# Kernel tuning notes

Measured on AMD Instinct MI355X. Metric: run time of the kernel, lower is better.

The kernel has to match this reference:

```python
import jax, jax.numpy as jnp
import numpy as np

B, D_IN, HID, DEPTH = 16384, 128, 16, 8
N_INNER = 2 ** DEPTH - 1   # 255
N_LEAF = 2 ** DEPTH        # 256


def setup_inputs() -> dict:
    key = jax.random.key(0)
    ks = jax.random.split(key, 4)
    x = jax.random.normal(ks[0], (B, D_IN), jnp.float32)
    # Batched per-inner-node tiny MLP parameters (PyTorch stores one Sequential per node;
    # we stack them along a leading node axis so the math is identical but vectorized).
    W1 = jax.random.normal(ks[1], (N_INNER, D_IN, HID), jnp.float32) / np.sqrt(D_IN).astype(np.float32)
    b1 = jnp.zeros((N_INNER, HID), jnp.float32)
    W2 = jax.random.normal(ks[2], (N_INNER, HID), jnp.float32) / np.sqrt(HID).astype(np.float32)
    b2 = jnp.zeros((N_INNER,), jnp.float32)
    leaf = jax.random.normal(ks[3], (N_LEAF, 1), jnp.float32) * 0.1
    return {"x": x, "W1": W1, "b1": b1, "W2": W2, "b2": b2, "leaf": leaf}


def reference(x, W1, b1, W2, b2, leaf):
    b = x.shape[0]
    depth = int(np.log2(leaf.shape[0]))
    # All inner-node gates in one batched GEMM: p[b, n] = sigmoid(W2_n . relu(W1_n^T x_b + b1_n) + b2_n)
    h1 = jax.nn.relu(jnp.einsum('bi,nih->bnh', x, W1) + b1[None])  # [B, N_inner, hid]
    p = jax.nn.sigmoid(jnp.einsum('bnh,nh->bn', h1, W2) + b2[None])  # [B, N_inner]

    # Level-by-level probability propagation (heap-ordered nodes):
    # children of node j are 2j+1 (left, mass*(1-p)) and 2j+2 (right, mass*p).
    r = jnp.ones((b, 1), x.dtype)
    levels = []
    for l in range(depth):
        levels.append(r)
        pl = p[:, 2 ** l - 1: 2 ** (l + 1) - 1]  # probs of nodes at level l, [B, 2^l]
        # interleave (left, right) so child ordering matches heap indexing
        r = jnp.stack([r * (1.0 - pl), r * pl], axis=-1).reshape(b, 2 ** (l + 1))
    node_reach = jnp.concatenate(levels, axis=1)  # [B, N_inner]
    path_probs = r                                 # [B, N_leaf]

    h = (path_probs @ leaf)[:, 0]                  # [B]
    return (h, path_probs, p, node_reach)
```

## Files before the change

### kernel.cpp

```cpp
#include <hip/hip_runtime.h>

#define BATCH 16384
#define DIN   128
#define HIDN  16
#define NNODE 255
#define NLEAF 256

typedef _Float16 half8 __attribute__((ext_vector_type(8)));
typedef float   float4v __attribute__((ext_vector_type(4)));

__global__ __launch_bounds__(256) void k_pack_x(const float* __restrict__ x, half8* __restrict__ xp) {
    int gid  = blockIdx.x * 256 + threadIdx.x;
    int lane = gid & 63;
    int kc   = (gid >> 6) & 3;
    int bt   = gid >> 8;
    const float4* src = (const float4*)(x + (size_t)(bt * 16 + (lane & 15)) * DIN + kc * 32 + ((lane >> 4) * 8));
    float4 v0 = src[0], v1 = src[1];
    half8 v;
    v[0] = (_Float16)v0.x; v[1] = (_Float16)v0.y; v[2] = (_Float16)v0.z; v[3] = (_Float16)v0.w;
    v[4] = (_Float16)v1.x; v[5] = (_Float16)v1.y; v[6] = (_Float16)v1.z; v[7] = (_Float16)v1.w;
    xp[gid] = v;
}

__global__ __launch_bounds__(256) void k_pack_w1(const float* __restrict__ w1, half8* __restrict__ w1p) {
    __shared__ float w[DIN * 17];
    int n = blockIdx.x;
    int t = threadIdx.x;
    const float4* src = (const float4*)(w1 + (size_t)n * (DIN * HIDN)) + t * 2;
    float4 a0 = src[0], a1 = src[1];
    int base = t * 8;
#pragma unroll
    for (int e = 0; e < 4; ++e) {
        int idx0 = base + e, idx1 = base + 4 + e;
        float v0 = (&a0.x)[e], v1 = (&a1.x)[e];
        w[(idx0 >> 4) * 17 + (idx0 & 15)] = v0;
        w[(idx1 >> 4) * 17 + (idx1 & 15)] = v1;
    }
    __syncthreads();
    int L  = t & 63;
    int kc = t >> 6;
    int m  = L & 15;
    int k0 = kc * 32 + (L >> 4) * 8;
    half8 v;
#pragma unroll
    for (int j = 0; j < 8; ++j) v[j] = (_Float16)w[(k0 + j) * 17 + m];
    w1p[(size_t)n * 256 + t] = v;
}

__global__ __launch_bounds__(256, 4) void k_mlp(const half8* __restrict__ xp, const half8* __restrict__ w1p,
                                                const float* __restrict__ b1, const float* __restrict__ w2,
                                                const float* __restrict__ b2, float* __restrict__ p_ws) {
    int wave = threadIdx.x >> 6;
    int lane = threadIdx.x & 63;
    int q    = lane >> 4;
    int c    = lane & 15;
    int bt0  = blockIdx.x * 16 + wave * 4;
    int n0   = blockIdx.y * 15;

    half8 bq[4][4];
#pragma unroll
    for (int t = 0; t < 4; ++t)
#pragma unroll
        for (int kc = 0; kc < 4; ++kc)
            bq[t][kc] = xp[(size_t)((bt0 + t) * 4 + kc) * 64 + lane];
    asm volatile("" ::: "memory");

    for (int i = 0; i < 15; ++i) {
        int n = n0 + i;
        half8 a[4];
#pragma unroll
        for (int kc = 0; kc < 4; ++kc) a[kc] = w1p[(size_t)(n * 4 + kc) * 64 + lane];
        float4 b1f = ((const float4*)(b1 + n * HIDN))[q];
        float4 w2f = ((const float4*)(w2 + n * HIDN))[q];
        float  b2v = b2[n];
#pragma unroll
        for (int t = 0; t < 4; ++t) {
            float4v acc = {b1f.x, b1f.y, b1f.z, b1f.w};
#pragma unroll
            for (int kc = 0; kc < 4; ++kc)
                acc = __builtin_amdgcn_mfma_f32_16x16x32_f16(a[kc], bq[t][kc], acc, 0, 0, 0);
            float s = fmaf(fmaxf(acc[0], 0.f), w2f.x,
                      fmaf(fmaxf(acc[1], 0.f), w2f.y,
                      fmaf(fmaxf(acc[2], 0.f), w2f.z,
                           fmaxf(acc[3], 0.f) * w2f.w)));
            s += __shfl_xor(s, 16, 64);
            s += __shfl_xor(s, 32, 64);
            float logit = s + b2v;
            float pv = __builtin_amdgcn_rcpf(1.f + __builtin_amdgcn_exp2f(-1.44269504088896f * logit));
            if (lane < 16)
                p_ws[(size_t)n * BATCH + (bt0 + t) * 16 + c] = pv;
        }
    }
}

__global__ __launch_bounds__(256) void k_tree(const float* __restrict__ p_ws, const float* __restrict__ leaf,
                                              float* __restrict__ h_out, float* __restrict__ pp_out,
                                              float* __restrict__ p_out, float* __restrict__ nr_out) {
    __shared__ float sp[32][NNODE + 2];
    int wv   = threadIdx.x >> 6;
    int lane = threadIdx.x & 63;
    int b0   = blockIdx.x * 32;
    int t    = threadIdx.x;

    for (int i = 0; i < 32; ++i) {
        int idx = i * 256 + t;
        if (idx < NNODE * 32) {
            int n = idx >> 5, bl = idx & 31;
            sp[bl][n] = p_ws[(size_t)n * BATCH + b0 + bl];
        }
    }
    __syncthreads();

    for (int r = 0; r < 32; ++r)
        if (t < NNODE)
            p_out[(size_t)(b0 + r) * NNODE + t] = sp[r][t];

    for (int rr = 0; rr < 8; ++rr) {
        int i = wv * 8 + rr;
        int b = b0 + i;
        const float* P = &sp[i][0];
        float* nr = nr_out + (size_t)b * NNODE;

        float pref = 1.f;
#pragma unroll
        for (int l = 0; l < 6; ++l) {
            if ((lane & ((1 << (6 - l)) - 1)) == 0) nr[(1 << l) - 1 + (lane >> (6 - l))] = pref;
            float pv  = P[(1 << l) - 1 + (lane >> (6 - l))];
            int  bit  = (lane >> (5 - l)) & 1;
            pref *= bit ? pv : (1.f - pv);
        }
        nr[63 + lane] = pref;
        float p6 = P[63 + lane];
        float pl = pref * (1.f - p6);
        float pr = pref * p6;
        nr[127 + 2 * lane] = pl;
        nr[128 + 2 * lane] = pr;
        float p7a = P[127 + 2 * lane];
        float p7b = P[128 + 2 * lane];
        float4 pp;
        pp.x = pl * (1.f - p7a);
        pp.y = pl * p7a;
        pp.z = pr * (1.f - p7b);
        pp.w = pr * p7b;
        *(float4*)(pp_out + (size_t)b * NLEAF + 4 * lane) = pp;
        const float4 lf = *(const float4*)(leaf + 4 * lane);
        float hs = pp.x * lf.x + pp.y * lf.y + pp.z * lf.z + pp.w * lf.w;
#pragma unroll
        for (int off = 1; off < 64; off <<= 1) hs += __shfl_xor(hs, off, 64);
        if (lane == 0) h_out[b] = hs;
    }
}

extern "C" void kernel_launch(void* const* d_in, const int* in_sizes, int n_in,
                              void* d_out, int out_size, void* d_ws, size_t ws_size,
                              hipStream_t stream) {
    const float* x    = (const float*)d_in[0];
    const float* W1   = (const float*)d_in[1];
    const float* b1   = (const float*)d_in[2];
    const float* W2   = (const float*)d_in[3];
    const float* b2   = (const float*)d_in[4];
    const float* leaf = (const float*)d_in[5];

    float* out    = (float*)d_out;
    float* h_out  = out;
    float* pp_out = out + BATCH;
    float* p_out  = pp_out + (size_t)BATCH * NLEAF;
    float* nr_out = p_out + (size_t)BATCH * NNODE;

    half8* xp   = (half8*)d_ws;
    half8* w1p  = xp + (size_t)1024 * 4 * 64;
    float* p_ws = (float*)(w1p + (size_t)NNODE * 256);

    hipLaunchKernelGGL(k_pack_x,  dim3(1024),  dim3(256), 0, stream, x, xp);
    hipLaunchKernelGGL(k_pack_w1, dim3(NNODE), dim3(256), 0, stream, W1, w1p);
    hipLaunchKernelGGL(k_mlp,     dim3(64, 17), dim3(256), 0, stream, xp, w1p, b1, W2, b2, p_ws);
    hipLaunchKernelGGL(k_tree,    dim3(BATCH / 32), dim3(256), 0, stream,
                       p_ws, leaf, h_out, pp_out, p_out, nr_out);
}
```

Before: 133.0 us.

## Swap MFMA operand roles, DPP row reductions, move sigmoid to tree kernel, smaller tiles

k_mlp swaps the MFMA A/B operands so each lane holds four batch rows for one hidden unit. The W2 dot product becomes a DPP row reduction over 16 lanes, replacing cross-row shuffles, and each row writes a float4 of logits. Each wave now handles 2 batch tiles instead of 4, the grid doubles, and launch bounds rise to 5 blocks per CU. The sigmoid moves into k_tree, which now works on 16 rows per block, doubling its grid and shrinking shared memory to raise parallelism. The trade-off is more redundant W1 loads per batch tile and more blocks to schedule.

```diff
diff --git a/kernel.cpp b/kernel.cpp
--- a/kernel.cpp
+++ b/kernel.cpp
@@ -5,9 +5,19 @@
 #define HIDN  16
 #define NNODE 255
 #define NLEAF 256
+#define TR    16
 
 typedef _Float16 half8 __attribute__((ext_vector_type(8)));
 typedef float   float4v __attribute__((ext_vector_type(4)));
+
+__device__ __forceinline__ float row_reduce16(float x) {
+    union U { float f; int i; } u, v;
+    u.f = x; v.i = __builtin_amdgcn_update_dpp(0, u.i, 0x128, 0xF, 0xF, true); x += v.f;
+    u.f = x; v.i = __builtin_amdgcn_update_dpp(0, u.i, 0x124, 0xF, 0xF, true); x += v.f;
+    u.f = x; v.i = __builtin_amdgcn_update_dpp(0, u.i, 0x122, 0xF, 0xF, true); x += v.f;
+    u.f = x; v.i = __builtin_amdgcn_update_dpp(0, u.i, 0x121, 0xF, 0xF, true); x += v.f;
+    return x;
+}
 
 __global__ __launch_bounds__(256) void k_pack_x(const float* __restrict__ x, half8* __restrict__ xp) {
     int gid  = blockIdx.x * 256 + threadIdx.x;
@@ -47,48 +57,50 @@
     w1p[(size_t)n * 256 + t] = v;
 }
 
-__global__ __launch_bounds__(256, 4) void k_mlp(const half8* __restrict__ xp, const half8* __restrict__ w1p,
+__global__ __launch_bounds__(256, 5) void k_mlp(const half8* __restrict__ xp, const half8* __restrict__ w1p,
                                                 const float* __restrict__ b1, const float* __restrict__ w2,
                                                 const float* __restrict__ b2, float* __restrict__ p_ws) {
-    int wave = threadIdx.x >> 6;
+    int wv   = threadIdx.x >> 6;
     int lane = threadIdx.x & 63;
-    int q    = lane >> 4;
-    int c    = lane & 15;
-    int bt0  = blockIdx.x * 16 + wave * 4;
+    int rg   = lane >> 4;
+    int hc   = lane & 15;
+    int bt0  = blockIdx.x * 8 + wv * 2;
     int n0   = blockIdx.y * 15;
 
-    half8 bq[4][4];
+    half8 xa[2][4];
 #pragma unroll
-    for (int t = 0; t < 4; ++t)
+    for (int t = 0; t < 2; ++t)
 #pragma unroll
         for (int kc = 0; kc < 4; ++kc)
-            bq[t][kc] = xp[(size_t)((bt0 + t) * 4 + kc) * 64 + lane];
+            xa[t][kc] = xp[(size_t)((bt0 + t) * 4 + kc) * 64 + lane];
     asm volatile("" ::: "memory");
 
     for (int i = 0; i < 15; ++i) {
         int n = n0 + i;
-        half8 a[4];
+        half8 wb[4];
 #pragma unroll
-        for (int kc = 0; kc < 4; ++kc) a[kc] = w1p[(size_t)(n * 4 + kc) * 64 + lane];
-        float4 b1f = ((const float4*)(b1 + n * HIDN))[q];
-        float4 w2f = ((const float4*)(w2 + n * HIDN))[q];
-        float  b2v = b2[n];
+        for (int kc = 0; kc < 4; ++kc) wb[kc] = w1p[(size_t)(n * 4 + kc) * 64 + lane];
+        float b1v = b1[n * HIDN + hc];
+        float w2v = w2[n * HIDN + hc];
+        float b2v = b2[n];
 #pragma unroll
-        for (int t = 0; t < 4; ++t) {
-            float4v acc = {b1f.x, b1f.y, b1f.z, b1f.w};
+        for (int t = 0; t < 2; ++t) {
+            float4v acc = {b1v, b1v, b1v, b1v};
 #pragma unroll
             for (int kc = 0; kc < 4; ++kc)
-                acc = __builtin_amdgcn_mfma_f32_16x16x32_f16(a[kc], bq[t][kc], acc, 0, 0, 0);
-            float s = fmaf(fmaxf(acc[0], 0.f), w2f.x,
-                      fmaf(fmaxf(acc[1], 0.f), w2f.y,
-                      fmaf(fmaxf(acc[2], 0.f), w2f.z,
-                           fmaxf(acc[3], 0.f) * w2f.w)));
-            s += __shfl_xor(s, 16, 64);
-            s += __shfl_xor(s, 32, 64);
-            float logit = s + b2v;
-            float pv = __builtin_amdgcn_rcpf(1.f + __builtin_amdgcn_exp2f(-1.44269504088896f * logit));
-            if (lane < 16)
-                p_ws[(size_t)n * BATCH + (bt0 + t) * 16 + c] = pv;
+                acc = __builtin_amdgcn_mfma_f32_16x16x32_f16(xa[t][kc], wb[kc], acc, 0, 0, 0);
+            float s0 = fmaxf(acc[0], 0.f) * w2v;
+            float s1 = fmaxf(acc[1], 0.f) * w2v;
+            float s2 = fmaxf(acc[2], 0.f) * w2v;
+            float s3 = fmaxf(acc[3], 0.f) * w2v;
+            s0 = row_reduce16(s0);
+            s1 = row_reduce16(s1);
+            s2 = row_reduce16(s2);
+            s3 = row_reduce16(s3);
+            if (hc == 0) {
+                float4 o = {s0 + b2v, s1 + b2v, s2 + b2v, s3 + b2v};
+                *(float4*)(p_ws + (size_t)n * BATCH + (bt0 + t) * 16 + rg * 4) = o;
+            }
         }
     }
 }
@@ -96,27 +108,29 @@
 __global__ __launch_bounds__(256) void k_tree(const float* __restrict__ p_ws, const float* __restrict__ leaf,
                                               float* __restrict__ h_out, float* __restrict__ pp_out,
                                               float* __restrict__ p_out, float* __restrict__ nr_out) {
-    __shared__ float sp[32][NNODE + 2];
+    __shared__ float sp[TR][NNODE + 2];
     int wv   = threadIdx.x >> 6;
     int lane = threadIdx.x & 63;
-    int b0   = blockIdx.x * 32;
+    int b0   = blockIdx.x * TR;
     int t    = threadIdx.x;
 
-    for (int i = 0; i < 32; ++i) {
+#pragma unroll
+    for (int i = 0; i < 16; ++i) {
         int idx = i * 256 + t;
-        if (idx < NNODE * 32) {
-            int n = idx >> 5, bl = idx & 31;
-            sp[bl][n] = p_ws[(size_t)n * BATCH + b0 + bl];
+        if (idx < NNODE * TR) {
+            int n = idx >> 4, bl = idx & 15;
+            float lg = p_ws[(size_t)n * BATCH + b0 + bl];
+            sp[bl][n] = __builtin_amdgcn_rcpf(1.f + __builtin_amdgcn_exp2f(-1.44269504088896f * lg));
         }
     }
     __syncthreads();
 
-    for (int r = 0; r < 32; ++r)
+    for (int r = 0; r < TR; ++r)
         if (t < NNODE)
             p_out[(size_t)(b0 + r) * NNODE + t] = sp[r][t];
 
-    for (int rr = 0; rr < 8; ++rr) {
-        int i = wv * 8 + rr;
+    for (int rr = 0; rr < 4; ++rr) {
+        int i = wv * 4 + rr;
         int b = b0 + i;
         const float* P = &sp[i][0];
         float* nr = nr_out + (size_t)b * NNODE;
@@ -173,7 +187,7 @@
 
     hipLaunchKernelGGL(k_pack_x,  dim3(1024),  dim3(256), 0, stream, x, xp);
     hipLaunchKernelGGL(k_pack_w1, dim3(NNODE), dim3(256), 0, stream, W1, w1p);
-    hipLaunchKernelGGL(k_mlp,     dim3(64, 17), dim3(256), 0, stream, xp, w1p, b1, W2, b2, p_ws);
-    hipLaunchKernelGGL(k_tree,    dim3(BATCH / 32), dim3(256), 0, stream,
+    hipLaunchKernelGGL(k_mlp,     dim3(128, 17), dim3(256), 0, stream, xp, w1p, b1, W2, b2, p_ws);
+    hipLaunchKernelGGL(k_tree,    dim3(BATCH / TR), dim3(256), 0, stream,
                        p_ws, leaf, h_out, pp_out, p_out, nr_out);
 }
```

Result: no change. 131.5 us (-1.1%).

## Merge pack kernels, use MFMA for second layer, move sigmoid into tree kernel

Applied to the files above, without the earlier changes.

Merges the x and W1 packing kernels into one launch, which also converts W2 to fp16. The second MLP layer's reduction (relu times W2 plus two cross-lane shuffles) becomes a 16x16x16 fp16 MFMA seeded with b2, and the kernel now stores raw logits. The sigmoid moves into the tree kernel's load phase, and that kernel now handles 16 rows per block instead of 32, doubling the block count. The MFMA path rounds the ReLU activations and W2 to fp16, which adds precision loss.

```diff
diff --git a/kernel.cpp b/kernel.cpp
--- a/kernel.cpp
+++ b/kernel.cpp
@@ -5,56 +5,60 @@
 #define HIDN  16
 #define NNODE 255
 #define NLEAF 256
+#define TR    16
 
 typedef _Float16 half8 __attribute__((ext_vector_type(8)));
+typedef _Float16 half4 __attribute__((ext_vector_type(4)));
 typedef float   float4v __attribute__((ext_vector_type(4)));
 
-__global__ __launch_bounds__(256) void k_pack_x(const float* __restrict__ x, half8* __restrict__ xp) {
-    int gid  = blockIdx.x * 256 + threadIdx.x;
-    int lane = gid & 63;
-    int kc   = (gid >> 6) & 3;
-    int bt   = gid >> 8;
-    const float4* src = (const float4*)(x + (size_t)(bt * 16 + (lane & 15)) * DIN + kc * 32 + ((lane >> 4) * 8));
-    float4 v0 = src[0], v1 = src[1];
-    half8 v;
-    v[0] = (_Float16)v0.x; v[1] = (_Float16)v0.y; v[2] = (_Float16)v0.z; v[3] = (_Float16)v0.w;
-    v[4] = (_Float16)v1.x; v[5] = (_Float16)v1.y; v[6] = (_Float16)v1.z; v[7] = (_Float16)v1.w;
-    xp[gid] = v;
-}
-
-__global__ __launch_bounds__(256) void k_pack_w1(const float* __restrict__ w1, half8* __restrict__ w1p) {
+__global__ __launch_bounds__(256) void k_pack(const float* __restrict__ x, const float* __restrict__ w1,
+                                              const float* __restrict__ w2,
+                                              half8* __restrict__ xp, half8* __restrict__ w1p,
+                                              _Float16* __restrict__ w2h) {
     __shared__ float w[DIN * 17];
-    int n = blockIdx.x;
     int t = threadIdx.x;
-    const float4* src = (const float4*)(w1 + (size_t)n * (DIN * HIDN)) + t * 2;
-    float4 a0 = src[0], a1 = src[1];
-    int base = t * 8;
+    if (blockIdx.x < 1024) {
+        int gid  = blockIdx.x * 256 + t;
+        int lane = gid & 63;
+        int kc   = (gid >> 6) & 3;
+        int bt   = gid >> 8;
+        const float4* src = (const float4*)(x + (size_t)(bt * 16 + (lane & 15)) * DIN + kc * 32 + ((lane >> 4) * 8));
+        float4 v0 = src[0], v1 = src[1];
+        half8 v;
+        v[0] = (_Float16)v0.x; v[1] = (_Float16)v0.y; v[2] = (_Float16)v0.z; v[3] = (_Float16)v0.w;
+        v[4] = (_Float16)v1.x; v[5] = (_Float16)v1.y; v[6] = (_Float16)v1.z; v[7] = (_Float16)v1.w;
+        xp[gid] = v;
+    } else {
+        int n = blockIdx.x - 1024;
+        const float4* src = (const float4*)(w1 + (size_t)n * (DIN * HIDN)) + t * 2;
+        float4 a0 = src[0], a1 = src[1];
+        int base = t * 8;
 #pragma unroll
-    for (int e = 0; e < 4; ++e) {
-        int idx0 = base + e, idx1 = base + 4 + e;
-        float v0 = (&a0.x)[e], v1 = (&a1.x)[e];
-        w[(idx0 >> 4) * 17 + (idx0 & 15)] = v0;
-        w[(idx1 >> 4) * 17 + (idx1 & 15)] = v1;
+        for (int e = 0; e < 4; ++e) {
+            int idx0 = base + e, idx1 = base + 4 + e;
+            w[(idx0 >> 4) * 17 + (idx0 & 15)] = (&a0.x)[e];
+            w[(idx1 >> 4) * 17 + (idx1 & 15)] = (&a1.x)[e];
+        }
+        __syncthreads();
+        int L  = t & 63;
+        int kc = t >> 6;
+        int m  = L & 15;
+        int k0 = kc * 32 + (L >> 4) * 8;
+        half8 v;
+#pragma unroll
+        for (int j = 0; j < 8; ++j) v[j] = (_Float16)w[(k0 + j) * 17 + m];
+        w1p[(size_t)n * 256 + t] = v;
+        if (t < HIDN) w2h[n * HIDN + t] = (_Float16)w2[n * HIDN + t];
     }
-    __syncthreads();
-    int L  = t & 63;
-    int kc = t >> 6;
-    int m  = L & 15;
-    int k0 = kc * 32 + (L >> 4) * 8;
-    half8 v;
-#pragma unroll
-    for (int j = 0; j < 8; ++j) v[j] = (_Float16)w[(k0 + j) * 17 + m];
-    w1p[(size_t)n * 256 + t] = v;
 }
 
 __global__ __launch_bounds__(256, 4) void k_mlp(const half8* __restrict__ xp, const half8* __restrict__ w1p,
-                                                const float* __restrict__ b1, const float* __restrict__ w2,
+                                                const float* __restrict__ b1, const _Float16* __restrict__ w2h,
                                                 const float* __restrict__ b2, float* __restrict__ p_ws) {
-    int wave = threadIdx.x >> 6;
+    int wv   = threadIdx.x >> 6;
     int lane = threadIdx.x & 63;
     int q    = lane >> 4;
-    int c    = lane & 15;
-    int bt0  = blockIdx.x * 16 + wave * 4;
+    int bt0  = blockIdx.x * 16 + wv * 4;
     int n0   = blockIdx.y * 15;
 
     half8 bq[4][4];
@@ -71,7 +75,7 @@
 #pragma unroll
         for (int kc = 0; kc < 4; ++kc) a[kc] = w1p[(size_t)(n * 4 + kc) * 64 + lane];
         float4 b1f = ((const float4*)(b1 + n * HIDN))[q];
-        float4 w2f = ((const float4*)(w2 + n * HIDN))[q];
+        half4  a2  = *(const half4*)(w2h + n * HIDN + q * 4);
         float  b2v = b2[n];
 #pragma unroll
         for (int t = 0; t < 4; ++t) {
@@ -79,16 +83,13 @@
 #pragma unroll
             for (int kc = 0; kc < 4; ++kc)
                 acc = __builtin_amdgcn_mfma_f32_16x16x32_f16(a[kc], bq[t][kc], acc, 0, 0, 0);
-            float s = fmaf(fmaxf(acc[0], 0.f), w2f.x,
-                      fmaf(fmaxf(acc[1], 0.f), w2f.y,
-                      fmaf(fmaxf(acc[2], 0.f), w2f.z,
-                           fmaxf(acc[3], 0.f) * w2f.w)));
-            s += __shfl_xor(s, 16, 64);
-            s += __shfl_xor(s, 32, 64);
-            float logit = s + b2v;
-            float pv = __builtin_amdgcn_rcpf(1.f + __builtin_amdgcn_exp2f(-1.44269504088896f * logit));
+            half4 rb;
+#pragma unroll
+            for (int r = 0; r < 4; ++r) rb[r] = (_Float16)fmaxf(acc[r], 0.f);
+            float4v acc2 = {b2v, b2v, b2v, b2v};
+            acc2 = __builtin_amdgcn_mfma_f32_16x16x16f16(a2, rb, acc2, 0, 0, 0);
             if (lane < 16)
-                p_ws[(size_t)n * BATCH + (bt0 + t) * 16 + c] = pv;
+                p_ws[(size_t)n * BATCH + (bt0 + t) * 16 + lane] = acc2[0];
         }
     }
 }
@@ -96,27 +97,29 @@
 __global__ __launch_bounds__(256) void k_tree(const float* __restrict__ p_ws, const float* __restrict__ leaf,
                                               float* __restrict__ h_out, float* __restrict__ pp_out,
                                               float* __restrict__ p_out, float* __restrict__ nr_out) {
-    __shared__ float sp[32][NNODE + 2];
+    __shared__ float sp[TR][NNODE + 2];
     int wv   = threadIdx.x >> 6;
     int lane = threadIdx.x & 63;
-    int b0   = blockIdx.x * 32;
+    int b0   = blockIdx.x * TR;
     int t    = threadIdx.x;
 
-    for (int i = 0; i < 32; ++i) {
+#pragma unroll
+    for (int i = 0; i < 16; ++i) {
         int idx = i * 256 + t;
-        if (idx < NNODE * 32) {
-            int n = idx >> 5, bl = idx & 31;
-            sp[bl][n] = p_ws[(size_t)n * BATCH + b0 + bl];
+        if (idx < NNODE * TR) {
+            int n = idx >> 4, bl = idx & 15;
+            float lg = p_ws[(size_t)n * BATCH + b0 + bl];
+            sp[bl][n] = __builtin_amdgcn_rcpf(1.f + __builtin_amdgcn_exp2f(-1.44269504088896f * lg));
         }
     }
     __syncthreads();
 
-    for (int r = 0; r < 32; ++r)
+    for (int r = 0; r < TR; ++r)
         if (t < NNODE)
             p_out[(size_t)(b0 + r) * NNODE + t] = sp[r][t];
 
-    for (int rr = 0; rr < 8; ++rr) {
-        int i = wv * 8 + rr;
+    for (int rr = 0; rr < 4; ++rr) {
+        int i = wv * 4 + rr;
         int b = b0 + i;
         const float* P = &sp[i][0];
         float* nr = nr_out + (size_t)b * NNODE;
@@ -167,13 +170,13 @@
     float* p_out  = pp_out + (size_t)BATCH * NLEAF;
     float* nr_out = p_out + (size_t)BATCH * NNODE;
 
-    half8* xp   = (half8*)d_ws;
-    half8* w1p  = xp + (size_t)1024 * 4 * 64;
-    float* p_ws = (float*)(w1p + (size_t)NNODE * 256);
+    half8*    xp   = (half8*)d_ws;
+    half8*    w1p  = xp + (size_t)1024 * 4 * 64;
+    _Float16* w2h  = (_Float16*)(w1p + (size_t)NNODE * 256);
+    float*    p_ws = (float*)((char*)w2h + ((NNODE * HIDN * 2 + 255) & ~255));
 
-    hipLaunchKernelGGL(k_pack_x,  dim3(1024),  dim3(256), 0, stream, x, xp);
-    hipLaunchKernelGGL(k_pack_w1, dim3(NNODE), dim3(256), 0, stream, W1, w1p);
-    hipLaunchKernelGGL(k_mlp,     dim3(64, 17), dim3(256), 0, stream, xp, w1p, b1, W2, b2, p_ws);
-    hipLaunchKernelGGL(k_tree,    dim3(BATCH / 32), dim3(256), 0, stream,
+    hipLaunchKernelGGL(k_pack, dim3(1024 + NNODE), dim3(256), 0, stream, x, W1, W2, xp, w1p, w2h);
+    hipLaunchKernelGGL(k_mlp,  dim3(64, 17), dim3(256), 0, stream, xp, w1p, b1, w2h, b2, p_ws);
+    hipLaunchKernelGGL(k_tree, dim3(BATCH / TR), dim3(256), 0, stream,
                        p_ws, leaf, h_out, pp_out, p_out, nr_out);
 }
```

New measurement: 124.9 us. -6.1%, faster.
